# Performance work log

Measured on AMD Instinct MI355X. Metric: run time of the kernel, lower is better.

Reference implementation:

```python
import jax, jax.numpy as jnp
import numpy as np

NEG_SLOPE = 0.2  # DGL GATConv default negative_slope


def gat_conv(x, W, attn_l, attn_r, bias, src, dst, n_nodes):
    """DGL-style GATConv. x:[N,F_in], W:[F_in,H*D], attn_l/attn_r/bias:[H,D].
    Returns [N,H,D]."""
    H, D = attn_l.shape
    feat = (x @ W).reshape(n_nodes, H, D)            # projected features
    el = jnp.sum(feat * attn_l, axis=-1)              # [N,H]
    er = jnp.sum(feat * attn_r, axis=-1)              # [N,H]
    e = jax.nn.leaky_relu(el[src] + er[dst], NEG_SLOPE)  # [E,H] per-edge score
    # edge softmax over incoming edges of each dst node (numerically stable)
    m = jax.ops.segment_max(e, dst, num_segments=n_nodes)   # [N,H]
    a = jnp.exp(e - m[dst])
    denom = jax.ops.segment_sum(a, dst, num_segments=n_nodes)
    alpha = a / denom[dst]                            # [E,H]
    msg = feat[src] * alpha[..., None]                # [E,H,D]
    out = jax.ops.segment_sum(msg, dst, num_segments=n_nodes)  # [N,H,D]
    return out + bias


def setup_inputs() -> dict:
    key = jax.random.key(0)
    ks = jax.random.split(key, 12)
    N, E = 50000, 800000
    F_in, D1, H1, F_out = 128, 32, 4, 64
    h = jax.random.normal(ks[0], (N, F_in), dtype=jnp.float32)
    src = jax.random.randint(ks[1], (E,), 0, N, dtype=jnp.int32)
    dst = jax.random.randint(ks[2], (E,), 0, N, dtype=jnp.int32)
    s1 = 1.0 / np.sqrt(F_in)
    s2 = 1.0 / np.sqrt(H1 * D1)
    W1 = jax.random.normal(ks[3], (F_in, H1 * D1), dtype=jnp.float32) * s1
    al1 = jax.random.normal(ks[4], (H1, D1), dtype=jnp.float32) * s1
    ar1 = jax.random.normal(ks[5], (H1, D1), dtype=jnp.float32) * s1
    b1 = jnp.zeros((H1, D1), dtype=jnp.float32)
    W2 = jax.random.normal(ks[6], (H1 * D1, 1 * F_out), dtype=jnp.float32) * s2
    al2 = jax.random.normal(ks[7], (1, F_out), dtype=jnp.float32) * s2
    ar2 = jax.random.normal(ks[8], (1, F_out), dtype=jnp.float32) * s2
    b2 = jnp.zeros((1, F_out), dtype=jnp.float32)
    return {"h": h, "src": src, "dst": dst,
            "W1": W1, "al1": al1, "ar1": ar1, "b1": b1,
            "W2": W2, "al2": al2, "ar2": ar2, "b2": b2}


def reference(h, src, dst, W1, al1, ar1, b1, W2, al2, ar2, b2):
    N = h.shape[0]
    x = gat_conv(h, W1, al1, ar1, b1, src, dst, N)   # [N,H,D]
    x = jax.nn.relu(x.reshape(N, -1))                # flatten heads + ReLU
    # dropout(p=0.2) is identity in eval mode
    x = gat_conv(x, W2, al2, ar2, b2, src, dst, N)   # [N,1,F_out]
    return x.squeeze(1)
```

## Files before the change

### kernel.cpp

```cpp
#include <hip/hip_runtime.h>

#define NEG_SLOPE 0.2f
#define CH 4096
#define DCAP 2048

__device__ inline unsigned short f2bf(float f) {
    unsigned u = __float_as_uint(f);
    unsigned r = (u + 0x7FFFu + ((u >> 16) & 1u)) >> 16;
    return (unsigned short)r;
}
__device__ inline float bf2f(unsigned short s) {
    return __uint_as_float(((unsigned)s) << 16);
}
__device__ inline void wave_lds_fence() {
    asm volatile("s_waitcnt lgkmcnt(0)" ::: "memory");
}

__global__ __launch_bounds__(256) void bucketAB_kernel(const int* __restrict__ dst,
                                                       int* __restrict__ bucket_cnt,
                                                       int* __restrict__ bucket_base,
                                                       int* __restrict__ bucket_cursor,
                                                       int* __restrict__ row_start,
                                                       int N, int NB, int E) {
    __shared__ int lh[1024];
    __shared__ int psum[256];
    __shared__ int ticket_sh;
    const int tid = threadIdx.x;
    for (int i = tid; i < 1024; i += 256) lh[i] = 0;
    __syncthreads();
    const int base = blockIdx.x * CH;
    const int cnt = min(CH, E - base);
    for (int i = tid; i < cnt; i += 256) atomicAdd(&lh[dst[base + i] >> 6], 1);
    __syncthreads();
    for (int b = tid; b < NB; b += 256)
        if (lh[b]) atomicAdd(&bucket_cnt[b], lh[b]);
    __syncthreads();
    if (tid == 0) {
        __threadfence();
        ticket_sh = atomicAdd(&bucket_cnt[NB], 1);
    }
    __syncthreads();
    if (ticket_sh != (int)gridDim.x - 1) return;
    for (int i = tid; i < 1024; i += 256)
        lh[i] = (i < NB) ? atomicAdd(&bucket_cnt[i], 0) : 0;
    __syncthreads();
    int s0 = lh[tid * 4], s1 = lh[tid * 4 + 1], s2 = lh[tid * 4 + 2], s3 = lh[tid * 4 + 3];
    int tot = s0 + s1 + s2 + s3;
    psum[tid] = tot;
    __syncthreads();
    for (int off = 1; off < 256; off <<= 1) {
        int t = (tid >= off) ? psum[tid - off] : 0;
        __syncthreads();
        psum[tid] += t;
        __syncthreads();
    }
    int ebase = psum[tid] - tot;
    int e0 = ebase, e1 = ebase + s0, e2 = ebase + s0 + s1, e3 = ebase + s0 + s1 + s2;
    int i0 = tid * 4;
    if (i0 < NB)     { bucket_base[i0]     = e0; bucket_cursor[i0]     = e0; }
    if (i0 + 1 < NB) { bucket_base[i0 + 1] = e1; bucket_cursor[i0 + 1] = e1; }
    if (i0 + 2 < NB) { bucket_base[i0 + 2] = e2; bucket_cursor[i0 + 2] = e2; }
    if (i0 + 3 < NB) { bucket_base[i0 + 3] = e3; bucket_cursor[i0 + 3] = e3; }
    if (tid == 255) bucket_base[NB] = psum[255];
    if (tid == 0) row_start[N] = E;
}

__global__ __launch_bounds__(256) void csrC_gemm1_kernel(
    const int* __restrict__ src, const int* __restrict__ dst,
    int* __restrict__ bucket_cursor, unsigned* __restrict__ tmp, int E, int NB,
    int nchunks, const float* __restrict__ h, const float* __restrict__ W1,
    const float* __restrict__ al1, const float* __restrict__ ar1,
    unsigned short* __restrict__ feat1b, float* __restrict__ el1,
    float* __restrict__ er1, int N) {
    __shared__ __align__(16) int smem[8448];
    const int tid = threadIdx.x;
    if ((int)blockIdx.x < nchunks) {
        int* lh = smem;
        int* lex = smem + 1024;
        int* lcur = smem + 2048;
        int* gbase_sh = smem + 3072;
        int* psum = smem + 4096;
        unsigned* sortedv = (unsigned*)(smem + 4352);
        const int base_e = blockIdx.x * CH;
        const int cnt_e = min(CH, E - base_e);
        for (int i = tid; i < 1024; i += 256) lh[i] = 0;
        __syncthreads();
        for (int i = tid; i < cnt_e; i += 256) atomicAdd(&lh[dst[base_e + i] >> 6], 1);
        __syncthreads();
        int s0 = lh[tid * 4], s1 = lh[tid * 4 + 1], s2 = lh[tid * 4 + 2], s3 = lh[tid * 4 + 3];
        int tot = s0 + s1 + s2 + s3;
        psum[tid] = tot;
        __syncthreads();
        for (int off = 1; off < 256; off <<= 1) {
            int t = (tid >= off) ? psum[tid - off] : 0;
            __syncthreads();
            psum[tid] += t;
            __syncthreads();
        }
        int ebase = psum[tid] - tot;
        lex[tid * 4] = ebase;
        lex[tid * 4 + 1] = ebase + s0;
        lex[tid * 4 + 2] = ebase + s0 + s1;
        lex[tid * 4 + 3] = ebase + s0 + s1 + s2;
        __syncthreads();
        for (int b = tid; b < NB; b += 256) {
            int c = lh[b];
            gbase_sh[b] = c ? atomicAdd(&bucket_cursor[b], c) : 0;
            lcur[b] = 0;
        }
        __syncthreads();
        for (int i = tid; i < cnt_e; i += 256) {
            int e = base_e + i;
            int d = dst[e];
            unsigned b = (unsigned)d >> 6;
            int r = atomicAdd(&lcur[b], 1);
            sortedv[lex[b] + r] =
                (b << 22) | ((unsigned)(d & 63) << 16) | (unsigned)(src[e] & 0xFFFF);
        }
        __syncthreads();
        for (int i = tid; i < cnt_e; i += 256) {
            unsigned v = sortedv[i];
            int b = v >> 22;
            tmp[gbase_sh[b] + (i - lex[b])] = v;
        }
    } else {
        float* xs = (float*)smem;
        const int row0 = ((int)blockIdx.x - nchunks) * 64;
        {
            const float4* s4 = (const float4*)h;
            float4* d4 = (float4*)xs;
            int base4 = row0 * 32;
            int tot4 = N * 32;
            for (int i = tid; i < 2048; i += 256)
                if (base4 + i < tot4) d4[i] = s4[base4 + i];
        }
        __syncthreads();
        const int lane = tid & 31;
        const int c0 = lane * 4;
        const int r0 = (tid >> 5) * 8;
        float acc[8][4] = {};
#pragma unroll 4
        for (int k = 0; k < 128; ++k) {
            float4 w = *(const float4*)(W1 + k * 128 + c0);
#pragma unroll
            for (int r = 0; r < 8; ++r) {
                float x = xs[(r0 + r) * 128 + k];
                acc[r][0] = fmaf(x, w.x, acc[r][0]);
                acc[r][1] = fmaf(x, w.y, acc[r][1]);
                acc[r][2] = fmaf(x, w.z, acc[r][2]);
                acc[r][3] = fmaf(x, w.w, acc[r][3]);
            }
        }
        float4 alv = *(const float4*)(al1 + c0);
        float4 arv = *(const float4*)(ar1 + c0);
#pragma unroll
        for (int r = 0; r < 8; ++r) {
            int row = row0 + r0 + r;
            if (row < N) {
                ushort4 fb;
                fb.x = f2bf(acc[r][0]);
                fb.y = f2bf(acc[r][1]);
                fb.z = f2bf(acc[r][2]);
                fb.w = f2bf(acc[r][3]);
                *(ushort4*)(feat1b + (size_t)row * 128 + c0) = fb;
                float pl = acc[r][0] * alv.x + acc[r][1] * alv.y + acc[r][2] * alv.z +
                           acc[r][3] * alv.w;
                float pr = acc[r][0] * arv.x + acc[r][1] * arv.y + acc[r][2] * arv.z +
                           acc[r][3] * arv.w;
#pragma unroll
                for (int off = 4; off >= 1; off >>= 1) {
                    pl += __shfl_xor(pl, off, 32);
                    pr += __shfl_xor(pr, off, 32);
                }
                if ((lane & 7) == 0) {
                    el1[row * 4 + (lane >> 3)] = pl;
                    er1[row * 4 + (lane >> 3)] = pr;
                }
            }
        }
    }
}

__global__ __launch_bounds__(256) void sortgather1_kernel(
    const unsigned* __restrict__ tmp, const int* __restrict__ bucket_base,
    int* __restrict__ srcs, int* __restrict__ row_start,
    const float* __restrict__ el1, const float* __restrict__ er1,
    const unsigned short* __restrict__ feat1b, const float* __restrict__ b1,
    unsigned short* __restrict__ out1b, int N, int NB) {
    __shared__ unsigned sval[DCAP];
    __shared__ int ssrc[DCAP];
    __shared__ int dh[64], dex[64], dcur[64];
    __shared__ float a_sh[4][256];
    const int b = blockIdx.x;
    const int tid = threadIdx.x;
    const int gb = bucket_base[b], ge = bucket_base[b + 1];
    const int cnt = ge - gb;
    if (tid < 64) dh[tid] = 0;
    __syncthreads();
    const bool lds_ok = (cnt <= DCAP);
    if (lds_ok) {
        for (int i = tid; i < cnt; i += 256) {
            unsigned v = tmp[gb + i];
            sval[i] = v;
            atomicAdd(&dh[(v >> 16) & 63], 1);
        }
        __syncthreads();
        if (tid < 64) {
            int v = dh[tid], inc = v;
            for (int off = 1; off < 64; off <<= 1) {
                int t = __shfl_up(inc, off, 64);
                if (tid >= off) inc += t;
            }
            dex[tid] = inc - v;
            dcur[tid] = 0;
            int dglob = b * 64 + tid;
            if (dglob < N) row_start[dglob] = gb + inc - v;
        }
        __syncthreads();
        for (int i = tid; i < cnt; i += 256) {
            unsigned val = sval[i];
            int dl = (val >> 16) & 63;
            int r = atomicAdd(&dcur[dl], 1);
            ssrc[dex[dl] + r] = (int)(val & 0xFFFFu);
        }
        __syncthreads();
        for (int i = tid; i < cnt; i += 256) srcs[gb + i] = ssrc[i];
    } else {
        for (int i = tid; i < cnt; i += 256) atomicAdd(&dh[(tmp[gb + i] >> 16) & 63], 1);
        __syncthreads();
        if (tid < 64) {
            int v = dh[tid], inc = v;
            for (int off = 1; off < 64; off <<= 1) {
                int t = __shfl_up(inc, off, 64);
                if (tid >= off) inc += t;
            }
            dex[tid] = inc - v;
            dcur[tid] = 0;
            int dglob = b * 64 + tid;
            if (dglob < N) row_start[dglob] = gb + inc - v;
        }
        __syncthreads();
        for (int i = tid; i < cnt; i += 256) {
            unsigned val = tmp[gb + i];
            int dl = (val >> 16) & 63;
            int r = atomicAdd(&dcur[dl], 1);
            srcs[gb + dex[dl] + r] = (int)(val & 0xFFFFu);
        }
        __syncthreads();
    }
    const int w = tid >> 6;
    const int lane = tid & 63;
    const int half = lane >> 5;
    const int l32 = lane & 31;
    const int c0 = l32 * 4;
    const int hh = l32 >> 3;
    const int* sp = lds_ok ? (const int*)ssrc : (srcs + gb);
    for (int t = 0; t < 16; ++t) {
        const int dl = w * 16 + t;
        const int d = b * 64 + dl;
        if (d >= N) break;
        const int ebeg = dex[dl];
        const int ecnt = dh[dl];
        float4 er4 = *(const float4*)(er1 + (size_t)d * 4);
        float acc0 = 0.f, acc1 = 0.f, acc2 = 0.f, acc3 = 0.f;
        float bcc0 = 0.f, bcc1 = 0.f, bcc2 = 0.f, bcc3 = 0.f;
        float den = 0.f;
        for (int k0 = 0; k0 < ecnt; k0 += 64) {
            const int M = min(64, ecnt - k0);
            if (lane < M) {
                int s = sp[ebeg + k0 + lane];
                float4 el4 = *(const float4*)(el1 + (size_t)s * 4);
                float v0 = el4.x + er4.x;
                float v1 = el4.y + er4.y;
                float v2 = el4.z + er4.z;
                float v3 = el4.w + er4.w;
                v0 = v0 > 0.f ? v0 : NEG_SLOPE * v0;
                v1 = v1 > 0.f ? v1 : NEG_SLOPE * v1;
                v2 = v2 > 0.f ? v2 : NEG_SLOPE * v2;
                v3 = v3 > 0.f ? v3 : NEG_SLOPE * v3;
                a_sh[w][lane * 4 + 0] = __expf(v0);
                a_sh[w][lane * 4 + 1] = __expf(v1);
                a_sh[w][lane * 4 + 2] = __expf(v2);
                a_sh[w][lane * 4 + 3] = __expf(v3);
            }
            wave_lds_fence();
            int e = half;
            for (; e + 2 < M; e += 4) {
                int s0 = sp[ebeg + k0 + e], s1 = sp[ebeg + k0 + e + 2];
                float a0 = a_sh[w][e * 4 + hh];
                float a1 = a_sh[w][(e + 2) * 4 + hh];
                ushort4 f0 = *(const ushort4*)(feat1b + (size_t)s0 * 128 + c0);
                ushort4 f1 = *(const ushort4*)(feat1b + (size_t)s1 * 128 + c0);
                den += a0 + a1;
                acc0 = fmaf(bf2f(f0.x), a0, acc0);
                acc1 = fmaf(bf2f(f0.y), a0, acc1);
                acc2 = fmaf(bf2f(f0.z), a0, acc2);
                acc3 = fmaf(bf2f(f0.w), a0, acc3);
                bcc0 = fmaf(bf2f(f1.x), a1, bcc0);
                bcc1 = fmaf(bf2f(f1.y), a1, bcc1);
                bcc2 = fmaf(bf2f(f1.z), a1, bcc2);
                bcc3 = fmaf(bf2f(f1.w), a1, bcc3);
            }
            if (e < M) {
                int s0 = sp[ebeg + k0 + e];
                float a0 = a_sh[w][e * 4 + hh];
                ushort4 f0 = *(const ushort4*)(feat1b + (size_t)s0 * 128 + c0);
                den += a0;
                acc0 = fmaf(bf2f(f0.x), a0, acc0);
                acc1 = fmaf(bf2f(f0.y), a0, acc1);
                acc2 = fmaf(bf2f(f0.z), a0, acc2);
                acc3 = fmaf(bf2f(f0.w), a0, acc3);
            }
            wave_lds_fence();
        }
        acc0 += bcc0;
        acc1 += bcc1;
        acc2 += bcc2;
        acc3 += bcc3;
        acc0 += __shfl_xor(acc0, 32, 64);
        acc1 += __shfl_xor(acc1, 32, 64);
        acc2 += __shfl_xor(acc2, 32, 64);
        acc3 += __shfl_xor(acc3, 32, 64);
        den += __shfl_xor(den, 32, 64);
        if (half == 0) {
            float inv = (ecnt > 0) ? 1.f / den : 0.f;
            float4 bv = *(const float4*)(b1 + c0);
            ushort4 o;
            o.x = f2bf(fmaxf(acc0 * inv + bv.x, 0.f));
            o.y = f2bf(fmaxf(acc1 * inv + bv.y, 0.f));
            o.z = f2bf(fmaxf(acc2 * inv + bv.z, 0.f));
            o.w = f2bf(fmaxf(acc3 * inv + bv.w, 0.f));
            *(ushort4*)(out1b + (size_t)d * 128 + c0) = o;
        }
    }
}

__global__ __launch_bounds__(256) void gemm2_fused(const unsigned short* __restrict__ out1b,
                                                   const float* __restrict__ W2,
                                                   const float* __restrict__ al2,
                                                   const float* __restrict__ ar2,
                                                   unsigned short* __restrict__ feat2b,
                                                   float* __restrict__ el2,
                                                   float* __restrict__ er2, int N) {
    __shared__ float xs[128 * 128];
    const int tid = threadIdx.x;
    const int row0 = blockIdx.x * 128;
    {
        const uint4* s8 = (const uint4*)out1b;
        int base8 = row0 * 16;
        int tot8 = N * 16;
        for (int i = tid; i < 2048; i += 256)
            if (base8 + i < tot8) {
                uint4 v = s8[base8 + i];
                float* o = xs + i * 8;
                o[0] = bf2f((unsigned short)(v.x & 0xFFFF));
                o[1] = bf2f((unsigned short)(v.x >> 16));
                o[2] = bf2f((unsigned short)(v.y & 0xFFFF));
                o[3] = bf2f((unsigned short)(v.y >> 16));
                o[4] = bf2f((unsigned short)(v.z & 0xFFFF));
                o[5] = bf2f((unsigned short)(v.z >> 16));
                o[6] = bf2f((unsigned short)(v.w & 0xFFFF));
                o[7] = bf2f((unsigned short)(v.w >> 16));
            }
    }
    __syncthreads();
    const int lane = tid & 15;
    const int c0 = lane * 4;
    const int r0 = (tid >> 4) * 8;
    float acc[8][4] = {};
#pragma unroll 4
    for (int k = 0; k < 128; ++k) {
        float4 w = *(const float4*)(W2 + k * 64 + c0);
#pragma unroll
        for (int r = 0; r < 8; ++r) {
            float x = xs[(r0 + r) * 128 + k];
            acc[r][0] = fmaf(x, w.x, acc[r][0]);
            acc[r][1] = fmaf(x, w.y, acc[r][1]);
            acc[r][2] = fmaf(x, w.z, acc[r][2]);
            acc[r][3] = fmaf(x, w.w, acc[r][3]);
        }
    }
    float4 alv = *(const float4*)(al2 + c0);
    float4 arv = *(const float4*)(ar2 + c0);
#pragma unroll
    for (int r = 0; r < 8; ++r) {
        int row = row0 + r0 + r;
        if (row < N) {
            ushort4 fb;
            fb.x = f2bf(acc[r][0]);
            fb.y = f2bf(acc[r][1]);
            fb.z = f2bf(acc[r][2]);
            fb.w = f2bf(acc[r][3]);
            *(ushort4*)(feat2b + (size_t)row * 64 + c0) = fb;
            float pl = acc[r][0] * alv.x + acc[r][1] * alv.y + acc[r][2] * alv.z +
                       acc[r][3] * alv.w;
            float pr = acc[r][0] * arv.x + acc[r][1] * arv.y + acc[r][2] * arv.z +
                       acc[r][3] * arv.w;
#pragma unroll
            for (int off = 8; off >= 1; off >>= 1) {
                pl += __shfl_xor(pl, off, 16);
                pr += __shfl_xor(pr, off, 16);
            }
            if (lane == 0) {
                el2[row] = pl;
                er2[row] = pr;
            }
        }
    }
}

__global__ __launch_bounds__(256) void gather2_kernel(const int* __restrict__ row_start,
                                                      const int* __restrict__ srcs,
                                                      const float* __restrict__ el2,
                                                      const float* __restrict__ er2,
                                                      const unsigned short* __restrict__ feat2b,
                                                      const float* __restrict__ b2,
                                                      float* __restrict__ out2, int N) {
    __shared__ int s_sh[4][64];
    __shared__ float a_sh[4][64];
    const int tid = threadIdx.x;
    const int w = tid >> 6;
    const int lane = tid & 63;
    const int d = blockIdx.x * 4 + w;
    if (d >= N) return;
    const int beg = row_start[d], end = row_start[d + 1];
    const int half = lane >> 5;
    const int l32 = lane & 31;
    const int c0 = l32 * 2;
    const float er_d = er2[d];
    float acc0 = 0.f, acc1 = 0.f, bcc0 = 0.f, bcc1 = 0.f, den = 0.f;
    for (int k0 = beg; k0 < end; k0 += 64) {
        const int M = min(64, end - k0);
        if (lane < M) {
            int s = srcs[k0 + lane];
            s_sh[w][lane] = s;
            float v = el2[s] + er_d;
            v = v > 0.f ? v : NEG_SLOPE * v;
            a_sh[w][lane] = __expf(v);
        }
        wave_lds_fence();
        int e = half;
        for (; e + 2 < M; e += 4) {
            int s0 = s_sh[w][e], s1 = s_sh[w][e + 2];
            float a0 = a_sh[w][e], a1 = a_sh[w][e + 2];
            ushort2 f0 = *(const ushort2*)(feat2b + (size_t)s0 * 64 + c0);
            ushort2 f1 = *(const ushort2*)(feat2b + (size_t)s1 * 64 + c0);
            den += a0 + a1;
            acc0 = fmaf(bf2f(f0.x), a0, acc0);
            acc1 = fmaf(bf2f(f0.y), a0, acc1);
            bcc0 = fmaf(bf2f(f1.x), a1, bcc0);
            bcc1 = fmaf(bf2f(f1.y), a1, bcc1);
        }
        if (e < M) {
            int s0 = s_sh[w][e];
            float a0 = a_sh[w][e];
            ushort2 f0 = *(const ushort2*)(feat2b + (size_t)s0 * 64 + c0);
            den += a0;
            acc0 = fmaf(bf2f(f0.x), a0, acc0);
            acc1 = fmaf(bf2f(f0.y), a0, acc1);
        }
        wave_lds_fence();
    }
    acc0 += bcc0;
    acc1 += bcc1;
    acc0 += __shfl_xor(acc0, 32, 64);
    acc1 += __shfl_xor(acc1, 32, 64);
    den += __shfl_xor(den, 32, 64);
    if (half == 0) {
        float inv = (end > beg) ? 1.f / den : 0.f;
        *(float2*)(out2 + (size_t)d * 64 + c0) =
            make_float2(acc0 * inv + b2[c0], acc1 * inv + b2[c0 + 1]);
    }
}

extern "C" void kernel_launch(void* const* d_in, const int* in_sizes, int n_in,
                              void* d_out, int out_size, void* d_ws, size_t ws_size,
                              hipStream_t stream) {
    const float* h   = (const float*)d_in[0];
    const int*   src = (const int*)d_in[1];
    const int*   dst = (const int*)d_in[2];
    const float* W1  = (const float*)d_in[3];
    const float* al1 = (const float*)d_in[4];
    const float* ar1 = (const float*)d_in[5];
    const float* b1  = (const float*)d_in[6];
    const float* W2  = (const float*)d_in[7];
    const float* al2 = (const float*)d_in[8];
    const float* ar2 = (const float*)d_in[9];
    const float* b2  = (const float*)d_in[10];

    const int N = in_sizes[0] / 128;
    const int E = in_sizes[1];
    const int NB = (N + 63) >> 6;

    char* ws = (char*)d_ws;
    size_t off = 0;
    auto alloc = [&](size_t elems) -> void* {
        void* p = (void*)(ws + off);
        off += ((elems * 4 + 255) / 256) * 256;
        return p;
    };
    int* bucket_cnt    = (int*)alloc(NB + 1);
    int* bucket_base   = (int*)alloc(NB + 1);
    int* bucket_cursor = (int*)alloc(NB);
    unsigned* tmp      = (unsigned*)alloc(E);
    int* srcs          = (int*)alloc(E);
    int* row_start     = (int*)alloc(N + 1);
    float* el1   = (float*)alloc((size_t)N * 4);
    float* er1   = (float*)alloc((size_t)N * 4);
    unsigned short* feat1b = (unsigned short*)alloc((size_t)N * 64);
    unsigned short* out1b  = (unsigned short*)alloc((size_t)N * 64);
    float* el2   = (float*)alloc(N);
    float* er2   = (float*)alloc(N);
    unsigned short* feat2b = (unsigned short*)alloc((size_t)N * 32);
    float* out2  = (float*)d_out;

    const int nchunks = (E + CH - 1) / CH;
    const int gemm1_blocks = (N + 63) / 64;

    hipMemsetAsync(bucket_cnt, 0, (size_t)(NB + 1) * 4, stream);
    bucketAB_kernel<<<nchunks, 256, 0, stream>>>(dst, bucket_cnt, bucket_base,
                                                 bucket_cursor, row_start, N, NB, E);
    csrC_gemm1_kernel<<<nchunks + gemm1_blocks, 256, 0, stream>>>(
        src, dst, bucket_cursor, tmp, E, NB, nchunks, h, W1, al1, ar1, feat1b, el1,
        er1, N);
    sortgather1_kernel<<<NB, 256, 0, stream>>>(tmp, bucket_base, srcs, row_start, el1,
                                               er1, feat1b, b1, out1b, N, NB);
    gemm2_fused<<<(N + 127) / 128, 256, 0, stream>>>(out1b, W2, al2, ar2, feat2b, el2,
                                                     er2, N);
    gather2_kernel<<<(N + 3) / 4, 256, 0, stream>>>(row_start, srcs, el2, er2, feat2b,
                                                    b2, out2, N);
}
```

Measured before the change: 242.2 us.

## Split fused bucket-sort and layer-1 gather into separate sort and gather kernels

```diff
diff --git a/kernel.cpp b/kernel.cpp
--- a/kernel.cpp
+++ b/kernel.cpp
@@ -181,24 +181,21 @@
     }
 }
 
-__global__ __launch_bounds__(256) void sortgather1_kernel(
-    const unsigned* __restrict__ tmp, const int* __restrict__ bucket_base,
-    int* __restrict__ srcs, int* __restrict__ row_start,
-    const float* __restrict__ el1, const float* __restrict__ er1,
-    const unsigned short* __restrict__ feat1b, const float* __restrict__ b1,
-    unsigned short* __restrict__ out1b, int N, int NB) {
+__global__ __launch_bounds__(256) void bucketD_kernel(const unsigned* __restrict__ tmp,
+                                                      const int* __restrict__ bucket_base,
+                                                      int* __restrict__ srcs,
+                                                      int* __restrict__ row_start,
+                                                      int N, int NB) {
     __shared__ unsigned sval[DCAP];
     __shared__ int ssrc[DCAP];
     __shared__ int dh[64], dex[64], dcur[64];
-    __shared__ float a_sh[4][256];
     const int b = blockIdx.x;
     const int tid = threadIdx.x;
     const int gb = bucket_base[b], ge = bucket_base[b + 1];
     const int cnt = ge - gb;
     if (tid < 64) dh[tid] = 0;
     __syncthreads();
-    const bool lds_ok = (cnt <= DCAP);
-    if (lds_ok) {
+    if (cnt <= DCAP) {
         for (int i = tid; i < cnt; i += 256) {
             unsigned v = tmp[gb + i];
             sval[i] = v;
@@ -245,92 +242,6 @@
             int dl = (val >> 16) & 63;
             int r = atomicAdd(&dcur[dl], 1);
             srcs[gb + dex[dl] + r] = (int)(val & 0xFFFFu);
-        }
-        __syncthreads();
-    }
-    const int w = tid >> 6;
-    const int lane = tid & 63;
-    const int half = lane >> 5;
-    const int l32 = lane & 31;
-    const int c0 = l32 * 4;
-    const int hh = l32 >> 3;
-    const int* sp = lds_ok ? (const int*)ssrc : (srcs + gb);
-    for (int t = 0; t < 16; ++t) {
-        const int dl = w * 16 + t;
-        const int d = b * 64 + dl;
-        if (d >= N) break;
-        const int ebeg = dex[dl];
-        const int ecnt = dh[dl];
-        float4 er4 = *(const float4*)(er1 + (size_t)d * 4);
-        float acc0 = 0.f, acc1 = 0.f, acc2 = 0.f, acc3 = 0.f;
-        float bcc0 = 0.f, bcc1 = 0.f, bcc2 = 0.f, bcc3 = 0.f;
-        float den = 0.f;
-        for (int k0 = 0; k0 < ecnt; k0 += 64) {
-            const int M = min(64, ecnt - k0);
-            if (lane < M) {
-                int s = sp[ebeg + k0 + lane];
-                float4 el4 = *(const float4*)(el1 + (size_t)s * 4);
-                float v0 = el4.x + er4.x;
-                float v1 = el4.y + er4.y;
-                float v2 = el4.z + er4.z;
-                float v3 = el4.w + er4.w;
-                v0 = v0 > 0.f ? v0 : NEG_SLOPE * v0;
-                v1 = v1 > 0.f ? v1 : NEG_SLOPE * v1;
-                v2 = v2 > 0.f ? v2 : NEG_SLOPE * v2;
-                v3 = v3 > 0.f ? v3 : NEG_SLOPE * v3;
-                a_sh[w][lane * 4 + 0] = __expf(v0);
-                a_sh[w][lane * 4 + 1] = __expf(v1);
-                a_sh[w][lane * 4 + 2] = __expf(v2);
-                a_sh[w][lane * 4 + 3] = __expf(v3);
-            }
-            wave_lds_fence();
-            int e = half;
-            for (; e + 2 < M; e += 4) {
-                int s0 = sp[ebeg + k0 + e], s1 = sp[ebeg + k0 + e + 2];
-                float a0 = a_sh[w][e * 4 + hh];
-                float a1 = a_sh[w][(e + 2) * 4 + hh];
-                ushort4 f0 = *(const ushort4*)(feat1b + (size_t)s0 * 128 + c0);
-                ushort4 f1 = *(const ushort4*)(feat1b + (size_t)s1 * 128 + c0);
-                den += a0 + a1;
-                acc0 = fmaf(bf2f(f0.x), a0, acc0);
-                acc1 = fmaf(bf2f(f0.y), a0, acc1);
-                acc2 = fmaf(bf2f(f0.z), a0, acc2);
-                acc3 = fmaf(bf2f(f0.w), a0, acc3);
-                bcc0 = fmaf(bf2f(f1.x), a1, bcc0);
-                bcc1 = fmaf(bf2f(f1.y), a1, bcc1);
-                bcc2 = fmaf(bf2f(f1.z), a1, bcc2);
-                bcc3 = fmaf(bf2f(f1.w), a1, bcc3);
-            }
-            if (e < M) {
-                int s0 = sp[ebeg + k0 + e];
-                float a0 = a_sh[w][e * 4 + hh];
-                ushort4 f0 = *(const ushort4*)(feat1b + (size_t)s0 * 128 + c0);
-                den += a0;
-                acc0 = fmaf(bf2f(f0.x), a0, acc0);
-                acc1 = fmaf(bf2f(f0.y), a0, acc1);
-                acc2 = fmaf(bf2f(f0.z), a0, acc2);
-                acc3 = fmaf(bf2f(f0.w), a0, acc3);
-            }
-            wave_lds_fence();
-        }
-        acc0 += bcc0;
-        acc1 += bcc1;
-        acc2 += bcc2;
-        acc3 += bcc3;
-        acc0 += __shfl_xor(acc0, 32, 64);
-        acc1 += __shfl_xor(acc1, 32, 64);
-        acc2 += __shfl_xor(acc2, 32, 64);
-        acc3 += __shfl_xor(acc3, 32, 64);
-        den += __shfl_xor(den, 32, 64);
-        if (half == 0) {
-            float inv = (ecnt > 0) ? 1.f / den : 0.f;
-            float4 bv = *(const float4*)(b1 + c0);
-            ushort4 o;
-            o.x = f2bf(fmaxf(acc0 * inv + bv.x, 0.f));
-            o.y = f2bf(fmaxf(acc1 * inv + bv.y, 0.f));
-            o.z = f2bf(fmaxf(acc2 * inv + bv.z, 0.f));
-            o.w = f2bf(fmaxf(acc3 * inv + bv.w, 0.f));
-            *(ushort4*)(out1b + (size_t)d * 128 + c0) = o;
         }
     }
 }
@@ -406,6 +317,100 @@
                 er2[row] = pr;
             }
         }
+    }
+}
+
+__global__ __launch_bounds__(256) void gather1_kernel(const int* __restrict__ row_start,
+                                                      const int* __restrict__ srcs,
+                                                      const float* __restrict__ el1,
+                                                      const float* __restrict__ er1,
+                                                      const unsigned short* __restrict__ feat1b,
+                                                      const float* __restrict__ b1,
+                                                      unsigned short* __restrict__ out1b,
+                                                      int N) {
+    __shared__ int s_sh[4][64];
+    __shared__ float a_sh[4][256];
+    const int tid = threadIdx.x;
+    const int w = tid >> 6;
+    const int lane = tid & 63;
+    const int d = blockIdx.x * 4 + w;
+    if (d >= N) return;
+    const int beg = row_start[d], end = row_start[d + 1];
+    const int half = lane >> 5;
+    const int l32 = lane & 31;
+    const int c0 = l32 * 4;
+    const int h = l32 >> 3;
+    float4 er4 = *(const float4*)(er1 + (size_t)d * 4);
+    float acc0 = 0.f, acc1 = 0.f, acc2 = 0.f, acc3 = 0.f;
+    float bcc0 = 0.f, bcc1 = 0.f, bcc2 = 0.f, bcc3 = 0.f;
+    float den = 0.f;
+    for (int k0 = beg; k0 < end; k0 += 64) {
+        const int M = min(64, end - k0);
+        if (lane < M) {
+            int s = srcs[k0 + lane];
+            s_sh[w][lane] = s;
+            float4 el4 = *(const float4*)(el1 + (size_t)s * 4);
+            float v0 = el4.x + er4.x;
+            float v1 = el4.y + er4.y;
+            float v2 = el4.z + er4.z;
+            float v3 = el4.w + er4.w;
+            v0 = v0 > 0.f ? v0 : NEG_SLOPE * v0;
+            v1 = v1 > 0.f ? v1 : NEG_SLOPE * v1;
+            v2 = v2 > 0.f ? v2 : NEG_SLOPE * v2;
+            v3 = v3 > 0.f ? v3 : NEG_SLOPE * v3;
+            a_sh[w][lane * 4 + 0] = __expf(v0);
+            a_sh[w][lane * 4 + 1] = __expf(v1);
+            a_sh[w][lane * 4 + 2] = __expf(v2);
+            a_sh[w][lane * 4 + 3] = __expf(v3);
+        }
+        wave_lds_fence();
+        int e = half;
+        for (; e + 2 < M; e += 4) {
+            int s0 = s_sh[w][e], s1 = s_sh[w][e + 2];
+            float a0 = a_sh[w][e * 4 + h];
+            float a1 = a_sh[w][(e + 2) * 4 + h];
+            ushort4 f0 = *(const ushort4*)(feat1b + (size_t)s0 * 128 + c0);
+            ushort4 f1 = *(const ushort4*)(feat1b + (size_t)s1 * 128 + c0);
+            den += a0 + a1;
+            acc0 = fmaf(bf2f(f0.x), a0, acc0);
+            acc1 = fmaf(bf2f(f0.y), a0, acc1);
+            acc2 = fmaf(bf2f(f0.z), a0, acc2);
+            acc3 = fmaf(bf2f(f0.w), a0, acc3);
+            bcc0 = fmaf(bf2f(f1.x), a1, bcc0);
+            bcc1 = fmaf(bf2f(f1.y), a1, bcc1);
+            bcc2 = fmaf(bf2f(f1.z), a1, bcc2);
+            bcc3 = fmaf(bf2f(f1.w), a1, bcc3);
+        }
+        if (e < M) {
+            int s0 = s_sh[w][e];
+            float a0 = a_sh[w][e * 4 + h];
+            ushort4 f0 = *(const ushort4*)(feat1b + (size_t)s0 * 128 + c0);
+            den += a0;
+            acc0 = fmaf(bf2f(f0.x), a0, acc0);
+            acc1 = fmaf(bf2f(f0.y), a0, acc1);
+            acc2 = fmaf(bf2f(f0.z), a0, acc2);
+            acc3 = fmaf(bf2f(f0.w), a0, acc3);
+        }
+        wave_lds_fence();
+    }
+    acc0 += bcc0;
+    acc1 += bcc1;
+    acc2 += bcc2;
+    acc3 += bcc3;
+    acc0 += __shfl_xor(acc0, 32, 64);
+    acc1 += __shfl_xor(acc1, 32, 64);
+    acc2 += __shfl_xor(acc2, 32, 64);
+    acc3 += __shfl_xor(acc3, 32, 64);
+    den += __shfl_xor(den, 32, 64);
+    if (half == 0) {
+        float inv = (end > beg) ? 1.f / den : 0.f;
+        float4 bv = *(const float4*)(b1 + c0);
+        ushort4 o;
+        o.x = f2bf(fmaxf(acc0 * inv + bv.x, 0.f));
+        o.y = f2bf(fmaxf(acc1 * inv + bv.y, 0.f));
+        o.z = f2bf(fmaxf(acc2 * inv + bv.z, 0.f));
+        o.w = f2bf(fmaxf(acc3 * inv + bv.w, 0.f));
+        *(ushort4*)(out1b + (size_t)d * 128 + c0) = o;
     }
 }
 
@@ -523,8 +528,11 @@
     csrC_gemm1_kernel<<<nchunks + gemm1_blocks, 256, 0, stream>>>(
         src, dst, bucket_cursor, tmp, E, NB, nchunks, h, W1, al1, ar1, feat1b, el1,
         er1, N);
-    sortgather1_kernel<<<NB, 256, 0, stream>>>(tmp, bucket_base, srcs, row_start, el1,
-                                               er1, feat1b, b1, out1b, N, NB);
+    bucketD_kernel<<<NB, 256, 0, stream>>>(tmp, bucket_base, srcs, row_start, N, NB);
+
+    gather1_kernel<<<(N + 3) / 4, 256, 0, stream>>>(row_start, srcs, el1, er1, feat1b,
+                                                    b1, out1b, N);
+
     gemm2_fused<<<(N + 127) / 128, 256, 0, stream>>>(out1b, W2, al2, ar2, feat2b, el2,
                                                      er2, N);
     gather2_kernel<<<(N + 3) / 4, 256, 0, stream>>>(row_start, srcs, el2, er2, feat2b,
```

Result: faster. 225.9 us (-6.7%).
